# Optimization experiments

Hardware: AMD Instinct MI355X
Metric: run time of the kernel (lower is better)

Reference implementation:

```python
import jax, jax.numpy as jnp
import numpy as np

C = 32
H = 8

def _layernorm(x, scale, bias, eps=1e-5):
    mu = jnp.mean(x, axis=-1, keepdims=True)
    var = jnp.mean(jnp.square(x - mu), axis=-1, keepdims=True)
    return (x - mu) * jax.lax.rsqrt(var + eps) * scale + bias


def setup_inputs() -> dict:
    key = jax.random.key(0)
    ks = jax.random.split(key, 10)
    B, s, i, j = 1, 128, 256, 256
    m = jax.random.normal(ks[0], (B, s, i, C), dtype=jnp.float32)
    z = jax.random.normal(ks[1], (B, i, j, C), dtype=jnp.float32)
    sd = 1.0 / np.sqrt(C)
    return {
        "m": m,
        "z": z,
        "ln_scale": jnp.ones((C,), jnp.float32),
        "ln_bias": jnp.zeros((C,), jnp.float32),
        "lnb_scale": jnp.ones((C,), jnp.float32),
        "lnb_bias": jnp.zeros((C,), jnp.float32),
        "wq": jax.random.normal(ks[2], (C, C * H), jnp.float32) * sd,
        "wk": jax.random.normal(ks[3], (C, C * H), jnp.float32) * sd,
        "wv": jax.random.normal(ks[4], (C, C * H), jnp.float32) * sd,
        "wb": jax.random.normal(ks[5], (C, H), jnp.float32) * sd,
        "wg": jax.random.normal(ks[6], (C, C * H), jnp.float32) * sd,
        "wo": jax.random.normal(ks[7], (C * H, C), jnp.float32) * (1.0 / np.sqrt(C * H)),
        "bo": jnp.zeros((C,), jnp.float32),
    }


def reference(m, z, ln_scale, ln_bias, lnb_scale, lnb_bias, wq, wk, wv, wb, wg, wo, bo):
    B, s, i, _ = m.shape
    j = z.shape[2]
    mn = _layernorm(m, ln_scale, ln_bias)                      # (B,s,i,c)
    q = (mn @ wq).reshape(B, s, i, H, C)                        # (B,s,i,h,c)
    k = (mn @ wk).reshape(B, s, i, H, C)
    v = (mn @ wv).reshape(B, s, i, H, C)
    gate = jax.nn.sigmoid(mn @ wg).reshape(B, s, i, H, C)       # (B,s,i,h,c)
    b = (_layernorm(z, lnb_scale, lnb_bias) @ wb)               # (B,i,j,h)
    a = jnp.einsum('bsihc,bsjhc->bsijh', q, k) * (C ** -0.5) + b[:, None]
    a = jax.nn.softmax(a, axis=-2)                              # softmax over j
    o = gate * jnp.einsum('bsijh,bsjhc->bsihc', a, v)
    o = o.reshape(B, s, i, H * C)
    return o @ wo + bo
```

## Files before the change

### kernel.cpp

```cpp
#include <hip/hip_runtime.h>

constexpr int NC = 32;
constexpr int NH = 8;
constexpr int NS = 128;
constexpr int NI = 256;
constexpr int NJ = 256;
constexpr float LN_EPS = 1e-5f;
constexpr float QSCALE = 0.17677669529663687f;
constexpr float LOG2E  = 1.4426950408889634f;

typedef __bf16 bf16x8 __attribute__((ext_vector_type(8)));
typedef __bf16 bf16x2 __attribute__((ext_vector_type(2)));
typedef float floatx4 __attribute__((ext_vector_type(4)));
typedef short short4v __attribute__((ext_vector_type(4)));

__device__ __forceinline__ float fexp2(float x) {
#if __has_builtin(__builtin_amdgcn_exp2f)
    return __builtin_amdgcn_exp2f(x);
#else
    return exp2f(x);
#endif
}
__device__ __forceinline__ float frcp(float x) {
#if __has_builtin(__builtin_amdgcn_rcpf)
    return __builtin_amdgcn_rcpf(x);
#else
    return 1.0f / x;
#endif
}
__device__ __forceinline__ unsigned pk2c(float a, float b) {
    union { bf16x2 v; unsigned u; } c;
    c.v = bf16x2{(__bf16)a, (__bf16)b};
    return c.u;
}
__device__ __forceinline__ unsigned pkbb(__bf16 a, __bf16 b) {
    union { bf16x2 v; unsigned u; } c;
    c.v = bf16x2{a, b};
    return c.u;
}

__device__ __forceinline__ int qkOff(int row, int chunk) {
    return row * 32 + ((chunk ^ ((row >> 1) & 3)) << 3);
}

__global__ __launch_bounds__(256) void biasprep_kernel(
    const float* __restrict__ z, const float* __restrict__ lnb_s,
    const float* __restrict__ lnb_b, const float* __restrict__ wb,
    const float* __restrict__ wq, const float* __restrict__ wk,
    const float* __restrict__ wv, const float* __restrict__ wg,
    const float* __restrict__ wo,
    float* __restrict__ bias32, unsigned short* __restrict__ wprep,
    unsigned short* __restrict__ wofrag)
{
    const int b = blockIdx.x;
    const int t = threadIdx.x;
    if (b < 256) {
        __shared__ float zL[256 * 33];
        const float4* src = (const float4*)(z + (size_t)b * NJ * NC);
#pragma unroll
        for (int k = 0; k < 8; ++k) {
            int idx = t + 256 * k;
            float4 v = src[idx];
            int f = idx * 4;
            int j = f >> 5, c = f & 31;
            zL[j * 33 + c]     = v.x; zL[j * 33 + c + 1] = v.y;
            zL[j * 33 + c + 2] = v.z; zL[j * 33 + c + 3] = v.w;
        }
        __syncthreads();

        float x[NC];
#pragma unroll
        for (int c = 0; c < NC; ++c) x[c] = zL[t * 33 + c];
        float mu = 0.f;
#pragma unroll
        for (int c = 0; c < NC; ++c) mu += x[c];
        mu *= (1.0f / NC);
        float var = 0.f;
#pragma unroll
        for (int c = 0; c < NC; ++c) { float d = x[c] - mu; var += d * d; }
        var *= (1.0f / NC);
        float rs = rsqrtf(var + LN_EPS);
        float acc[NH];
#pragma unroll
        for (int h = 0; h < NH; ++h) acc[h] = 0.f;
#pragma unroll
        for (int c = 0; c < NC; ++c) {
            float xn = (x[c] - mu) * rs * lnb_s[c] + lnb_b[c];
#pragma unroll
            for (int h = 0; h < NH; ++h) acc[h] += xn * wb[c * NH + h];
        }
        const int i = b;
        const int w_ = i >> 6, it = (i >> 4) & 3, lm = i & 15;
        const int jc = t >> 5, jt = (t >> 4) & 1, lq = (t >> 2) & 3, r = t & 3;
        const int base = jc * 8192 + w_ * 2048 + (jt * 4 + it) * 256
                       + (lq * 16 + lm) * 4 + r;
#pragma unroll
        for (int h = 0; h < NH; ++h)
            bias32[h * 65536 + base] = acc[h] * LOG2E;
    } else if (b < 272) {
        int g = (b - 256) * 256 + t;
        int p  = g >> 10;
        int h  = (g >> 7) & 7;
        int ct = (g >> 6) & 1;
        int l  = g & 63;
        const float* W = (p == 0) ? wq : (p == 1) ? wk : (p == 2) ? wv : wg;
        float scale = (p == 0) ? QSCALE * LOG2E : (p == 3) ? LOG2E : 1.0f;
        int col = 32 * h + 16 * ct + (l & 15);
        int r0  = 8 * (l >> 4);
        float v[8];
#pragma unroll
        for (int e = 0; e < 8; ++e) v[e] = W[(r0 + e) * 256 + col] * scale;
        uint4 u;
        u.x = pk2c(v[0], v[1]); u.y = pk2c(v[2], v[3]);
        u.z = pk2c(v[4], v[5]); u.w = pk2c(v[6], v[7]);
        *(uint4*)&wprep[g * 8] = u;
    } else {
        int g = (b - 272) * 256 + t;
        int tile = g >> 6;
        int l = g & 63;
        int kt = tile >> 1, nt = tile & 1;
        int r0 = kt * 32 + 8 * (l >> 4);
        int col = nt * 16 + (l & 15);
        float v[8];
#pragma unroll
        for (int e = 0; e < 8; ++e) v[e] = wo[(r0 + e) * 32 + col];
        uint4 u;
        u.x = pk2c(v[0], v[1]); u.y = pk2c(v[2], v[3]);
        u.z = pk2c(v[4], v[5]); u.w = pk2c(v[6], v[7]);
        *(uint4*)&wofrag[g * 8] = u;
    }
}

__global__ __launch_bounds__(256, 4) void attn_kernel(
    const float* __restrict__ m, const float* __restrict__ ln_s,
    const float* __restrict__ ln_b,
    const unsigned short* __restrict__ wprep,
    const float* __restrict__ bias32,
    unsigned short* __restrict__ attn16)
{
    __shared__ unsigned short KX[256 * 32];
    __shared__ unsigned short VF[32 * 256];

    const int t = threadIdx.x;
    const int h = blockIdx.x & 7;
    const int s = blockIdx.x >> 3;
    const int l = t & 63, w = t >> 6;
    const int lm = l & 15, lq = l >> 4;
    const int ibase = w * 64;
    const floatx4 zero = {0.f, 0.f, 0.f, 0.f};

    {
        const float4* mr = (const float4*)(m + ((size_t)s * NI + t) * NC);
        float x[NC];
#pragma unroll
        for (int k = 0; k < 8; ++k) {
            float4 v = mr[k];
            x[4*k] = v.x; x[4*k+1] = v.y; x[4*k+2] = v.z; x[4*k+3] = v.w;
        }
        float mu = 0.f;
#pragma unroll
        for (int c = 0; c < NC; ++c) mu += x[c];
        mu *= (1.0f / NC);
        float var = 0.f;
#pragma unroll
        for (int c = 0; c < NC; ++c) { float d = x[c] - mu; var += d * d; }
        var *= (1.0f / NC);
        float rs = rsqrtf(var + LN_EPS);
#pragma unroll
        for (int k = 0; k < 4; ++k) {
            uint4 u;
            u.x = pk2c((x[8*k+0]-mu)*rs*ln_s[8*k+0]+ln_b[8*k+0],
                       (x[8*k+1]-mu)*rs*ln_s[8*k+1]+ln_b[8*k+1]);
            u.y = pk2c((x[8*k+2]-mu)*rs*ln_s[8*k+2]+ln_b[8*k+2],
                       (x[8*k+3]-mu)*rs*ln_s[8*k+3]+ln_b[8*k+3]);
            u.z = pk2c((x[8*k+4]-mu)*rs*ln_s[8*k+4]+ln_b[8*k+4],
                       (x[8*k+5]-mu)*rs*ln_s[8*k+5]+ln_b[8*k+5]);
            u.w = pk2c((x[8*k+6]-mu)*rs*ln_s[8*k+6]+ln_b[8*k+6],
                       (x[8*k+7]-mu)*rs*ln_s[8*k+7]+ln_b[8*k+7]);
            *(uint4*)&KX[qkOff(t, k)] = u;
        }
    }

    const unsigned short* wp = wprep + ((size_t)h * 128 + l) * 8;
    bf16x8 wfQ[2], wfK[2], wfV[2];
#pragma unroll
    for (int ct = 0; ct < 2; ++ct) {
        wfQ[ct] = *(const bf16x8*)&wp[(0 * 1024 + ct * 64) * 8];
        wfK[ct] = *(const bf16x8*)&wp[(1 * 1024 + ct * 64) * 8];
        wfV[ct] = *(const bf16x8*)&wp[(2 * 1024 + ct * 64) * 8];
    }
    bf16x8 Xb[4];
#pragma unroll
    for (int it = 0; it < 4; ++it)
        Xb[it] = *(const bf16x8*)&KX[qkOff(ibase + it * 16 + lm, lq)];

#pragma unroll
    for (int it = 0; it < 4; ++it)
#pragma unroll
        for (int ct = 0; ct < 2; ++ct) {
            floatx4 d = __builtin_amdgcn_mfma_f32_16x16x32_bf16(wfQ[ct], Xb[it], zero, 0, 0, 0);
            uint2 u; u.x = pk2c(d[0], d[1]); u.y = pk2c(d[2], d[3]);
            int row = ibase + it * 16 + lm;
            *(uint2*)&KX[qkOff(row, 2 * ct + (lq >> 1)) + (lq & 1) * 4] = u;
        }
    bf16x8 Qb[4];
#pragma unroll
    for (int it = 0; it < 4; ++it)
        Qb[it] = *(const bf16x8*)&KX[qkOff(ibase + it * 16 + lm, lq)];

#pragma unroll
    for (int it = 0; it < 4; ++it)
#pragma unroll
        for (int ct = 0; ct < 2; ++ct) {
            floatx4 d = __builtin_amdgcn_mfma_f32_16x16x32_bf16(wfK[ct], Xb[it], zero, 0, 0, 0);
            uint2 u; u.x = pk2c(d[0], d[1]); u.y = pk2c(d[2], d[3]);
            int row = ibase + it * 16 + lm;
            *(uint2*)&KX[qkOff(row, 2 * ct + (lq >> 1)) + (lq & 1) * 4] = u;
        }

#pragma unroll
    for (int jt = 0; jt < 4; ++jt)
#pragma unroll
        for (int ct = 0; ct < 2; ++ct) {
            floatx4 d = __builtin_amdgcn_mfma_f32_16x16x32_bf16(Xb[jt], wfV[ct], zero, 0, 0, 0);
            uint2 u; u.x = pk2c(d[0], d[1]); u.y = pk2c(d[2], d[3]);
            int tile = (w * 4 + jt) * 2 + ct;
            *(uint2*)&VF[(tile * 64 + l) * 4] = u;
        }

    __syncthreads();

    floatx4 accO[2][4];
#pragma unroll
    for (int ct = 0; ct < 2; ++ct)
#pragma unroll
        for (int it = 0; it < 4; ++it) accO[ct][it] = zero;
    floatx4 accL[4];
#pragma unroll
    for (int it = 0; it < 4; ++it) accL[it] = zero;
    short4v onesB;
#pragma unroll
    for (int e = 0; e < 4; ++e) onesB[e] = (short)0x3F80;

    const float* bptr = bias32 + (size_t)h * 65536 + w * 2048 + l * 4;

    for (int jc = 0; jc < 8; ++jc) {
        const float* bj = bptr + jc * 8192;
#pragma unroll
        for (int jt = 0; jt < 2; ++jt) {
            bf16x8 Ka = *(const bf16x8*)&KX[qkOff(jc * 32 + jt * 16 + lm, lq)];
            const int J = jc * 2 + jt;
            short4v Vb0 = *(const short4v*)&VF[((J * 2 + 0) * 64 + l) * 4];
            short4v Vb1 = *(const short4v*)&VF[((J * 2 + 1) * 64 + l) * 4];
#pragma unroll
            for (int it = 0; it < 4; ++it) {
                floatx4 C = *(const floatx4*)(bj + (jt * 4 + it) * 256);
                floatx4 S = __builtin_amdgcn_mfma_f32_16x16x32_bf16(Ka, Qb[it], C, 0, 0, 0);
                union { unsigned u[2]; short4v s4; } pu;
                pu.u[0] = pkbb((__bf16)fexp2(S[0]), (__bf16)fexp2(S[1]));
                pu.u[1] = pkbb((__bf16)fexp2(S[2]), (__bf16)fexp2(S[3]));
                accO[0][it] = __builtin_amdgcn_mfma_f32_16x16x16bf16_1k(pu.s4, Vb0, accO[0][it], 0, 0, 0);
                accO[1][it] = __builtin_amdgcn_mfma_f32_16x16x16bf16_1k(pu.s4, Vb1, accO[1][it], 0, 0, 0);
                accL[it]    = __builtin_amdgcn_mfma_f32_16x16x16bf16_1k(pu.s4, onesB, accL[it], 0, 0, 0);
            }
        }
    }

    {
        bf16x8 wfG0 = *(const bf16x8*)&wp[(3 * 1024 + 0 * 64) * 8];
        bf16x8 wfG1 = *(const bf16x8*)&wp[(3 * 1024 + 1 * 64) * 8];
        __bf16* a16 = (__bf16*)attn16;
#pragma unroll
        for (int it = 0; it < 4; ++it) {
            floatx4 g0 = __builtin_amdgcn_mfma_f32_16x16x32_bf16(Xb[it], wfG0, zero, 0, 0, 0);
            floatx4 g1 = __builtin_amdgcn_mfma_f32_16x16x32_bf16(Xb[it], wfG1, zero, 0, 0, 0);
#pragma unroll
            for (int r = 0; r < 4; ++r) {
                const float inv = frcp(accL[it][r]);
                float o0 = accO[0][it][r] * inv * frcp(1.0f + fexp2(-g0[r]));
                float o1 = accO[1][it][r] * inv * frcp(1.0f + fexp2(-g1[r]));
                const size_t rowb = ((size_t)s * NI + ibase + it * 16 + lq * 4 + r) * 256 + h * 32;
                a16[rowb + lm]      = (__bf16)o0;
                a16[rowb + 16 + lm] = (__bf16)o1;
            }
        }
    }
}

__global__ __launch_bounds__(256) void proj_kernel(
    const unsigned short* __restrict__ attn16,
    const unsigned short* __restrict__ wofrag,
    const float* __restrict__ bo, float* __restrict__ out)
{
    const int t = threadIdx.x;
    const int l = t & 63, w = t >> 6;
    const int lm = l & 15, lq = l >> 4;
    const int row0 = blockIdx.x * 128 + w * 32;
    const floatx4 zero = {0.f, 0.f, 0.f, 0.f};

    floatx4 acc[2][2];
#pragma unroll
    for (int it = 0; it < 2; ++it)
#pragma unroll
        for (int nt = 0; nt < 2; ++nt) acc[it][nt] = zero;

#pragma unroll 2
    for (int kt = 0; kt < 8; ++kt) {
        bf16x8 a0 = *(const bf16x8*)&attn16[(size_t)(row0 + lm) * 256 + kt * 32 + lq * 8];
        bf16x8 a1 = *(const bf16x8*)&attn16[(size_t)(row0 + 16 + lm) * 256 + kt * 32 + lq * 8];
        bf16x8 b0 = *(const bf16x8*)&wofrag[((kt * 2 + 0) * 64 + l) * 8];
        bf16x8 b1 = *(const bf16x8*)&wofrag[((kt * 2 + 1) * 64 + l) * 8];
        acc[0][0] = __builtin_amdgcn_mfma_f32_16x16x32_bf16(a0, b0, acc[0][0], 0, 0, 0);
        acc[0][1] = __builtin_amdgcn_mfma_f32_16x16x32_bf16(a0, b1, acc[0][1], 0, 0, 0);
        acc[1][0] = __builtin_amdgcn_mfma_f32_16x16x32_bf16(a1, b0, acc[1][0], 0, 0, 0);
        acc[1][1] = __builtin_amdgcn_mfma_f32_16x16x32_bf16(a1, b1, acc[1][1], 0, 0, 0);
    }

    float bov[2] = {bo[lm], bo[16 + lm]};
#pragma unroll
    for (int it = 0; it < 2; ++it)
#pragma unroll
        for (int nt = 0; nt < 2; ++nt)
#pragma unroll
            for (int r = 0; r < 4; ++r)
                out[(size_t)(row0 + it * 16 + lq * 4 + r) * NC + nt * 16 + lm]
                    = acc[it][nt][r] + bov[nt];
}

extern "C" void kernel_launch(void* const* d_in, const int* in_sizes, int n_in,
                              void* d_out, int out_size, void* d_ws, size_t ws_size,
                              hipStream_t stream) {
    const float* m     = (const float*)d_in[0];
    const float* z     = (const float*)d_in[1];
    const float* ln_s  = (const float*)d_in[2];
    const float* ln_b  = (const float*)d_in[3];
    const float* lnb_s = (const float*)d_in[4];
    const float* lnb_b = (const float*)d_in[5];
    const float* wq    = (const float*)d_in[6];
    const float* wk    = (const float*)d_in[7];
    const float* wv    = (const float*)d_in[8];
    const float* wb    = (const float*)d_in[9];
    const float* wg    = (const float*)d_in[10];
    const float* wo    = (const float*)d_in[11];
    const float* bo    = (const float*)d_in[12];
    float* out = (float*)d_out;

    float* bias32 = (float*)d_ws;
    unsigned short* wprep  = (unsigned short*)((char*)d_ws + (2u << 20));
    unsigned short* wofrag = (unsigned short*)((char*)d_ws + (2u << 20) + 65536);
    unsigned short* attn16 = (unsigned short*)((char*)d_ws + (2u << 20) + 65536 + 16384);

    biasprep_kernel<<<276, 256, 0, stream>>>(z, lnb_s, lnb_b, wb, wq, wk, wv, wg,
                                             wo, bias32, wprep, wofrag);
    attn_kernel<<<NS * NH, 256, 0, stream>>>(m, ln_s, ln_b, wprep, bias32, attn16);
    proj_kernel<<<(NS * NI) / 128, 256, 0, stream>>>(attn16, wofrag, bo, out);
}
```

Before: 128.3 us.

## Restage P through LDS to use K=32 MFMA for PV and drop ones-MFMA row sums

The PV product changes from three 16x16x16 MFMAs per tile (two for V, one against a ones matrix for the softmax denominator) to two 16x16x32 MFMAs. The exponentiated scores are written to a per-wave swizzled LDS buffer and re-read in the layout the operand needs, and V is stored transposed with an XOR swizzle. Row sums are now accumulated in scalar registers and reduced with cross-lane shuffles. The output is transposed so each lane stores four contiguous bf16 values instead of scattered scalar stores. In exchange, each inner iteration adds an LDS write/read round-trip for P.

```diff
diff --git a/kernel.cpp b/kernel.cpp
--- a/kernel.cpp
+++ b/kernel.cpp
@@ -12,7 +12,6 @@
 typedef __bf16 bf16x8 __attribute__((ext_vector_type(8)));
 typedef __bf16 bf16x2 __attribute__((ext_vector_type(2)));
 typedef float floatx4 __attribute__((ext_vector_type(4)));
-typedef short short4v __attribute__((ext_vector_type(4)));
 
 __device__ __forceinline__ float fexp2(float x) {
 #if __has_builtin(__builtin_amdgcn_exp2f)
@@ -33,14 +32,15 @@
     c.v = bf16x2{(__bf16)a, (__bf16)b};
     return c.u;
 }
-__device__ __forceinline__ unsigned pkbb(__bf16 a, __bf16 b) {
-    union { bf16x2 v; unsigned u; } c;
-    c.v = bf16x2{a, b};
-    return c.u;
-}
 
 __device__ __forceinline__ int qkOff(int row, int chunk) {
     return row * 32 + ((chunk ^ ((row >> 1) & 3)) << 3);
+}
+__device__ __forceinline__ int vOff(int c, int chunk) {
+    return c * 256 + ((chunk ^ (c & 7)) << 3);
+}
+__device__ __forceinline__ int pOff(int wbase, int row, int chunk) {
+    return wbase + row * 32 + ((chunk ^ ((row >> 1) & 3)) << 3);
 }
 
 __global__ __launch_bounds__(256) void biasprep_kernel(
@@ -139,7 +139,8 @@
     unsigned short* __restrict__ attn16)
 {
     __shared__ unsigned short KX[256 * 32];
-    __shared__ unsigned short VF[32 * 256];
+    __shared__ unsigned short Vt[32 * 256];
+    __shared__ unsigned short Pbuf[4 * 512];
 
     const int t = threadIdx.x;
     const int h = blockIdx.x & 7;
@@ -147,6 +148,7 @@
     const int l = t & 63, w = t >> 6;
     const int lm = l & 15, lq = l >> 4;
     const int ibase = w * 64;
+    const int pwb = w * 512;
     const floatx4 zero = {0.f, 0.f, 0.f, 0.f};
 
     {
@@ -224,8 +226,9 @@
         for (int ct = 0; ct < 2; ++ct) {
             floatx4 d = __builtin_amdgcn_mfma_f32_16x16x32_bf16(Xb[jt], wfV[ct], zero, 0, 0, 0);
             uint2 u; u.x = pk2c(d[0], d[1]); u.y = pk2c(d[2], d[3]);
-            int tile = (w * 4 + jt) * 2 + ct;
-            *(uint2*)&VF[(tile * 64 + l) * 4] = u;
+            int c = ct * 16 + lm;
+            int chunk = 8 * w + 2 * jt + (lq >> 1);
+            *(uint2*)&Vt[vOff(c, chunk) + (lq & 1) * 4] = u;
         }
 
     __syncthreads();
@@ -235,53 +238,64 @@
     for (int ct = 0; ct < 2; ++ct)
 #pragma unroll
         for (int it = 0; it < 4; ++it) accO[ct][it] = zero;
-    floatx4 accL[4];
-#pragma unroll
-    for (int it = 0; it < 4; ++it) accL[it] = zero;
-    short4v onesB;
-#pragma unroll
-    for (int e = 0; e < 4; ++e) onesB[e] = (short)0x3F80;
+    float accLv[4] = {0.f, 0.f, 0.f, 0.f};
 
     const float* bptr = bias32 + (size_t)h * 65536 + w * 2048 + l * 4;
 
     for (int jc = 0; jc < 8; ++jc) {
         const float* bj = bptr + jc * 8192;
-#pragma unroll
-        for (int jt = 0; jt < 2; ++jt) {
-            bf16x8 Ka = *(const bf16x8*)&KX[qkOff(jc * 32 + jt * 16 + lm, lq)];
-            const int J = jc * 2 + jt;
-            short4v Vb0 = *(const short4v*)&VF[((J * 2 + 0) * 64 + l) * 4];
-            short4v Vb1 = *(const short4v*)&VF[((J * 2 + 1) * 64 + l) * 4];
-#pragma unroll
-            for (int it = 0; it < 4; ++it) {
-                floatx4 C = *(const floatx4*)(bj + (jt * 4 + it) * 256);
-                floatx4 S = __builtin_amdgcn_mfma_f32_16x16x32_bf16(Ka, Qb[it], C, 0, 0, 0);
-                union { unsigned u[2]; short4v s4; } pu;
-                pu.u[0] = pkbb((__bf16)fexp2(S[0]), (__bf16)fexp2(S[1]));
-                pu.u[1] = pkbb((__bf16)fexp2(S[2]), (__bf16)fexp2(S[3]));
-                accO[0][it] = __builtin_amdgcn_mfma_f32_16x16x16bf16_1k(pu.s4, Vb0, accO[0][it], 0, 0, 0);
-                accO[1][it] = __builtin_amdgcn_mfma_f32_16x16x16bf16_1k(pu.s4, Vb1, accO[1][it], 0, 0, 0);
-                accL[it]    = __builtin_amdgcn_mfma_f32_16x16x16bf16_1k(pu.s4, onesB, accL[it], 0, 0, 0);
-            }
+        bf16x8 Ka0 = *(const bf16x8*)&KX[qkOff(jc * 32 + lm, lq)];
+        bf16x8 Ka1 = *(const bf16x8*)&KX[qkOff(jc * 32 + 16 + lm, lq)];
+        bf16x8 Va0 = *(const bf16x8*)&Vt[vOff(lm, 4 * jc + lq)];
+        bf16x8 Va1 = *(const bf16x8*)&Vt[vOff(16 + lm, 4 * jc + lq)];
+#pragma unroll
+        for (int it = 0; it < 4; ++it) {
+            floatx4 C0 = *(const floatx4*)(bj + it * 256);
+            floatx4 S0 = __builtin_amdgcn_mfma_f32_16x16x32_bf16(Ka0, Qb[it], C0, 0, 0, 0);
+            floatx4 C1 = *(const floatx4*)(bj + (4 + it) * 256);
+            floatx4 S1 = __builtin_amdgcn_mfma_f32_16x16x32_bf16(Ka1, Qb[it], C1, 0, 0, 0);
+            float p0 = fexp2(S0[0]), p1 = fexp2(S0[1]);
+            float p2 = fexp2(S0[2]), p3 = fexp2(S0[3]);
+            float p4 = fexp2(S1[0]), p5 = fexp2(S1[1]);
+            float p6 = fexp2(S1[2]), p7 = fexp2(S1[3]);
+            accLv[it] += ((p0 + p1) + (p2 + p3)) + ((p4 + p5) + (p6 + p7));
+            uint2 u0; u0.x = pk2c(p0, p1); u0.y = pk2c(p2, p3);
+            uint2 u1; u1.x = pk2c(p4, p5); u1.y = pk2c(p6, p7);
+            *(uint2*)&Pbuf[pOff(pwb, lm, 0 + (lq >> 1)) + (lq & 1) * 4] = u0;
+            *(uint2*)&Pbuf[pOff(pwb, lm, 2 + (lq >> 1)) + (lq & 1) * 4] = u1;
+            bf16x8 Pb = *(const bf16x8*)&Pbuf[pOff(pwb, lm, lq)];
+            accO[0][it] = __builtin_amdgcn_mfma_f32_16x16x32_bf16(Va0, Pb, accO[0][it], 0, 0, 0);
+            accO[1][it] = __builtin_amdgcn_mfma_f32_16x16x32_bf16(Va1, Pb, accO[1][it], 0, 0, 0);
         }
     }
 
     {
         bf16x8 wfG0 = *(const bf16x8*)&wp[(3 * 1024 + 0 * 64) * 8];
         bf16x8 wfG1 = *(const bf16x8*)&wp[(3 * 1024 + 1 * 64) * 8];
-        __bf16* a16 = (__bf16*)attn16;
 #pragma unroll
         for (int it = 0; it < 4; ++it) {
-            floatx4 g0 = __builtin_amdgcn_mfma_f32_16x16x32_bf16(Xb[it], wfG0, zero, 0, 0, 0);
-            floatx4 g1 = __builtin_amdgcn_mfma_f32_16x16x32_bf16(Xb[it], wfG1, zero, 0, 0, 0);
-#pragma unroll
-            for (int r = 0; r < 4; ++r) {
-                const float inv = frcp(accL[it][r]);
-                float o0 = accO[0][it][r] * inv * frcp(1.0f + fexp2(-g0[r]));
-                float o1 = accO[1][it][r] * inv * frcp(1.0f + fexp2(-g1[r]));
-                const size_t rowb = ((size_t)s * NI + ibase + it * 16 + lq * 4 + r) * 256 + h * 32;
-                a16[rowb + lm]      = (__bf16)o0;
-                a16[rowb + 16 + lm] = (__bf16)o1;
+            float L = accLv[it];
+            L += __shfl_xor(L, 16, 64);
+            L += __shfl_xor(L, 32, 64);
+            const float inv = frcp(L);
+            floatx4 d0 = __builtin_amdgcn_mfma_f32_16x16x32_bf16(wfG0, Xb[it], zero, 0, 0, 0);
+            floatx4 d1 = __builtin_amdgcn_mfma_f32_16x16x32_bf16(wfG1, Xb[it], zero, 0, 0, 0);
+            const size_t rowb = ((size_t)s * NI + ibase + it * 16 + lm) * 256 + h * 32;
+            {
+                float o0 = accO[0][it][0] * inv * frcp(1.0f + fexp2(-d0[0]));
+                float o1 = accO[0][it][1] * inv * frcp(1.0f + fexp2(-d0[1]));
+                float o2 = accO[0][it][2] * inv * frcp(1.0f + fexp2(-d0[2]));
+                float o3 = accO[0][it][3] * inv * frcp(1.0f + fexp2(-d0[3]));
+                uint2 u; u.x = pk2c(o0, o1); u.y = pk2c(o2, o3);
+                *(uint2*)&attn16[rowb + 0 * 16 + lq * 4] = u;
+            }
+            {
+                float o0 = accO[1][it][0] * inv * frcp(1.0f + fexp2(-d1[0]));
+                float o1 = accO[1][it][1] * inv * frcp(1.0f + fexp2(-d1[1]));
+                float o2 = accO[1][it][2] * inv * frcp(1.0f + fexp2(-d1[2]));
+                float o3 = accO[1][it][3] * inv * frcp(1.0f + fexp2(-d1[3]));
+                uint2 u; u.x = pk2c(o0, o1); u.y = pk2c(o2, o3);
+                *(uint2*)&attn16[rowb + 1 * 16 + lq * 4] = u;
             }
         }
     }
```

Result: faster. 123.6 us (-3.6%).
